# Kernel tuning notes

Hardware: AMD Instinct MI355X
Metric: run time of the kernel (lower is better)

## Reference

```python
import jax, jax.numpy as jnp
import numpy as np

EMBED_DIM = 1024
NUM_HEADS = 16
HEAD_DIM = EMBED_DIM // NUM_HEADS
EPSILON = 0.01
C = 2.0 + EPSILON
SCORE_SCALE = 1.0
B, L = 2, 2048


def setup_inputs() -> dict:
    key = jax.random.key(0)
    k0, k1, k2, k3, k4 = jax.random.split(key, 5)
    x = jax.random.normal(k0, (B, L, EMBED_DIM), dtype=jnp.float32)
    # flax Linear kernels: (in, out)
    W_qkv = jax.random.normal(k1, (EMBED_DIM, 3 * EMBED_DIM), dtype=jnp.float32) / np.sqrt(EMBED_DIM)
    b_qkv = jnp.zeros((3 * EMBED_DIM,), dtype=jnp.float32)
    W_out = jax.random.normal(k2, (EMBED_DIM, EMBED_DIM), dtype=jnp.float32) / np.sqrt(EMBED_DIM)
    b_out = jnp.zeros((EMBED_DIM,), dtype=jnp.float32)
    return {"x": x, "W_qkv": W_qkv, "b_qkv": b_qkv, "W_out": W_out, "b_out": b_out}


def reference(x, W_qkv, b_qkv, W_out, b_out):
    Bb, Ll, E = x.shape
    qkv = x @ W_qkv + b_qkv                      # [B, L, 3E]
    q, k, v = jnp.split(qkv, 3, axis=-1)
    def to_heads(t):
        return t.reshape(Bb, Ll, NUM_HEADS, HEAD_DIM).transpose(0, 2, 1, 3)  # [B,H,L,D]
    q, k, v = to_heads(q), to_heads(k), to_heads(v)
    q_norm = q / jnp.linalg.norm(q, axis=-1, keepdims=True)
    k_norm = k / jnp.linalg.norm(k, axis=-1, keepdims=True)
    x_dot = jnp.einsum('bhid,bhjd->bhij', q_norm, k_norm)   # [B,H,L,L]
    scores = (x_dot ** 2) / (C - 2.0 * x_dot) * SCORE_SCALE
    mask = jnp.triu(jnp.ones((Ll, Ll), dtype=scores.dtype), k=1) * -1e9
    scores = scores + mask[None, None, :, :]
    attn = jax.nn.softmax(scores, axis=-1)
    out = jnp.einsum('bhij,bhjd->bhid', attn, v)            # [B,H,L,D]
    out = out.transpose(0, 2, 1, 3).reshape(Bb, Ll, E)
    return out @ W_out + b_out
```

## Files before the change

### kernel.cpp

```cpp
#include <hip/hip_runtime.h>
#include <cstdint>
#include <cstddef>

#define B_DIM 2
#define L_DIM 2048
#define E_DIM 1024
#define H_DIM 16
#define HD    64
#define M_ROWS (B_DIM * L_DIM)
#define QKV_N  (3 * E_DIM)
#define C_CONST 2.01f
#define NCH_BH 40
#define LOG2E 1.4426950408889634f
#define LN2   0.6931471805599453f

typedef unsigned short ushort_t;
typedef __attribute__((ext_vector_type(8))) short bf16x8;
typedef __attribute__((ext_vector_type(4))) float f32x4;

__device__ __forceinline__ unsigned int f2bf(float f) {
    union { float f; unsigned int u; } v; v.f = f;
    return (v.u + 0x7FFFu + ((v.u >> 16) & 1u)) >> 16;
}
__device__ __forceinline__ float bf2f_lo(unsigned int u) {
    union { unsigned int u; float f; } v; v.u = u << 16; return v.f;
}
__device__ __forceinline__ float bf2f_hi(unsigned int u) {
    union { unsigned int u; float f; } v; v.u = u & 0xffff0000u; return v.f;
}

__device__ __forceinline__ void gload16(const void* g, void* l) {
    __builtin_amdgcn_global_load_lds(
        (const __attribute__((address_space(1))) void*)g,
        (__attribute__((address_space(3))) void*)l, 16, 0, 0);
}

__device__ __forceinline__ void transpose_tile_dev(
    const float* __restrict__ in, ushort_t* __restrict__ out,
    int R, int Cn, int c0, int r0, int tid, float t[64][65])
{
    for (int idx = tid; idx < 4096; idx += 256) {
        const int r = idx >> 6, c = idx & 63;
        t[r][c] = in[(size_t)(r0 + r) * Cn + c0 + c];
    }
    __syncthreads();
    for (int idx = tid; idx < 4096; idx += 256) {
        const int c = idx >> 6, r = idx & 63;
        out[(size_t)(c0 + c) * R + r0 + r] = (ushort_t)f2bf(t[r][c]);
    }
}

__global__ __launch_bounds__(256) void prep_kernel(
    const float* __restrict__ x, ushort_t* __restrict__ xb,
    const float* __restrict__ Wqkv, ushort_t* __restrict__ WqkvT,
    const float* __restrict__ Wout, ushort_t* __restrict__ WoutT)
{
    __shared__ float t[64][65];
    const int bx = blockIdx.x;
    const int tid = threadIdx.x;
    if (bx < 4096) {
        const int i = bx * 256 + tid;
        const float4 v = ((const float4*)x)[i];
        uint2 p;
        p.x = f2bf(v.x) | (f2bf(v.y) << 16);
        p.y = f2bf(v.z) | (f2bf(v.w) << 16);
        ((uint2*)xb)[i] = p;
    } else if (bx < 4096 + 768) {
        const int idx = bx - 4096;
        transpose_tile_dev(Wqkv, WqkvT, E_DIM, QKV_N, (idx % 48) * 64, (idx / 48) * 64, tid, t);
    } else {
        const int idx = bx - 4864;
        transpose_tile_dev(Wout, WoutT, E_DIM, E_DIM, (idx & 15) * 64, (idx >> 4) * 64, tid, t);
    }
}

template<int NCOLS, int MODE>
__global__ __launch_bounds__(256) void gemm_bt_kernel(
    const ushort_t* __restrict__ A, const ushort_t* __restrict__ BT,
    const float* __restrict__ bias, float* __restrict__ outf,
    ushort_t* __restrict__ q16, ushort_t* __restrict__ k16,
    ushort_t* __restrict__ v16)
{
    __shared__ __align__(16) ushort_t Abuf[128 * 32];
    __shared__ __align__(16) ushort_t Bbuf[128 * 32];
    const int tid = threadIdx.x;
    const int wave = tid >> 6, lane = tid & 63;
    const int m0 = blockIdx.x * 128, n0 = blockIdx.y * 128;
    const int wr = (wave >> 1) * 64, wc = (wave & 1) * 64;
    const int g = lane >> 4, l15 = lane & 15;

    f32x4 acc[4][4];
    #pragma unroll
    for (int i = 0; i < 4; ++i)
        #pragma unroll
        for (int j = 0; j < 4; ++j) acc[i][j] = f32x4{0.f, 0.f, 0.f, 0.f};

    const int sr = tid >> 2;
    const int sc = (tid & 3) * 8;
    const ushort_t* Asrc0 = A + (size_t)(m0 + sr) * 1024 + sc;
    const ushort_t* Asrc1 = A + (size_t)(m0 + 64 + sr) * 1024 + sc;
    const ushort_t* Bsrc0 = BT + (size_t)(n0 + sr) * 1024 + sc;
    const ushort_t* Bsrc1 = BT + (size_t)(n0 + 64 + sr) * 1024 + sc;
    ushort_t* Adst0 = &Abuf[tid * 8];
    ushort_t* Adst1 = &Abuf[2048 + tid * 8];
    ushort_t* Bdst0 = &Bbuf[tid * 8];
    ushort_t* Bdst1 = &Bbuf[2048 + tid * 8];

    for (int k0 = 0; k0 < 1024; k0 += 32) {
        __syncthreads();
        gload16(Asrc0 + k0, Adst0);
        gload16(Asrc1 + k0, Adst1);
        gload16(Bsrc0 + k0, Bdst0);
        gload16(Bsrc1 + k0, Bdst1);
        __syncthreads();

        bf16x8 af[4];
        #pragma unroll
        for (int mt = 0; mt < 4; ++mt)
            af[mt] = *(const bf16x8*)&Abuf[(wr + mt * 16 + l15) * 32 + 8 * g];
        #pragma unroll
        for (int nt = 0; nt < 4; ++nt) {
            const bf16x8 bfr = *(const bf16x8*)&Bbuf[(wc + nt * 16 + l15) * 32 + 8 * g];
            #pragma unroll
            for (int mt = 0; mt < 4; ++mt)
                acc[mt][nt] = __builtin_amdgcn_mfma_f32_16x16x32_bf16(af[mt], bfr, acc[mt][nt], 0, 0, 0);
        }
    }

    if (MODE == 0) {
        const int nBase = n0 + wc;
        const int sel = nBase >> 10;
        const int h   = (nBase & 1023) >> 6;
        float bv[4];
        #pragma unroll
        for (int nt = 0; nt < 4; ++nt) bv[nt] = bias[nBase + nt * 16 + l15];

        if (sel <= 1) {
            ushort_t* dst16 = (sel == 0) ? q16 : k16;
            #pragma unroll
            for (int mt = 0; mt < 4; ++mt) {
                float val[4][4], ss[4] = {0.f, 0.f, 0.f, 0.f};
                #pragma unroll
                for (int nt = 0; nt < 4; ++nt)
                    #pragma unroll
                    for (int r = 0; r < 4; ++r) {
                        const float v = acc[mt][nt][r] + bv[nt];
                        val[nt][r] = v;
                        ss[r] = fmaf(v, v, ss[r]);
                    }
                #pragma unroll
                for (int r = 0; r < 4; ++r) {
                    float t = ss[r];
                    t += __shfl_xor(t, 1); t += __shfl_xor(t, 2);
                    t += __shfl_xor(t, 4); t += __shfl_xor(t, 8);
                    ss[r] = 1.0f / sqrtf(t);
                }
                #pragma unroll
                for (int r = 0; r < 4; ++r) {
                    const int m = m0 + wr + mt * 16 + 4 * g + r;
                    const int bb = m >> 11, ll = m & 2047;
                    ushort_t* base = dst16 + ((size_t)((bb * H_DIM + h) * L_DIM + ll)) * HD + l15;
                    #pragma unroll
                    for (int nt = 0; nt < 4; ++nt)
                        base[nt * 16] = (ushort_t)f2bf(val[nt][r] * ss[r]);
                }
            }
        } else {
            #pragma unroll
            for (int mt = 0; mt < 4; ++mt)
                #pragma unroll
                for (int r = 0; r < 4; ++r) {
                    const int m = m0 + wr + mt * 16 + 4 * g + r;
                    const int bb = m >> 11, ll = m & 2047;
                    ushort_t* base = v16 + ((size_t)((bb * H_DIM + h) * L_DIM + ll)) * HD + l15;
                    #pragma unroll
                    for (int nt = 0; nt < 4; ++nt)
                        base[nt * 16] = (ushort_t)f2bf(acc[mt][nt][r] + bv[nt]);
                }
        }
    } else {
        #pragma unroll
        for (int nt = 0; nt < 4; ++nt) {
            const int n = n0 + wc + nt * 16 + l15;
            const float bvv = bias[n];
            #pragma unroll
            for (int mt = 0; mt < 4; ++mt)
                #pragma unroll
                for (int r = 0; r < 4; ++r) {
                    const int m = m0 + wr + mt * 16 + 4 * g + r;
                    outf[(size_t)m * E_DIM + n] = acc[mt][nt][r] + bvv;
                }
        }
    }
}

__global__ __launch_bounds__(256) void vt_transpose_kernel(
    const ushort_t* __restrict__ vb, ushort_t* __restrict__ vt)
{
    __shared__ ushort_t t[64][68];
    const int kt = blockIdx.x, bh = blockIdx.y;
    const int tid = threadIdx.x;
    const ushort_t* src = vb + ((size_t)bh * L_DIM + kt * 64) * HD;
    #pragma unroll
    for (int p = 0; p < 16; ++p) {
        const int idx = tid + 256 * p;
        t[idx >> 6][idx & 63] = src[idx];
    }
    __syncthreads();
    ushort_t* dst = vt + (size_t)bh * HD * L_DIM + kt * 64;
    #pragma unroll
    for (int p = 0; p < 16; ++p) {
        const int idx = tid + 256 * p;
        const int d = idx >> 6, k = idx & 63;
        dst[(size_t)d * L_DIM + k] = t[k][d];
    }
}

__global__ __launch_bounds__(512) void attn_mfma_kernel(
    const ushort_t* __restrict__ qn, const ushort_t* __restrict__ kn,
    const ushort_t* __restrict__ vt,
    ushort_t* __restrict__ pO, float* __restrict__ pl, float* __restrict__ pm)
{
    __shared__ __align__(16) ushort_t Qs[128 * 64];
    __shared__ __align__(16) ushort_t Ks[2][64 * 64];
    __shared__ __align__(16) ushort_t Vs[2][64 * 64];

    int c = blockIdx.x, qtp = 0, s = 0;
    #pragma unroll
    for (int gg = 0; gg < 4; ++gg) {
        const int sz = 4 * (gg + 1);
        if (c < sz) { qtp = 4 * gg + c / (gg + 1); s = c - (c / (gg + 1)) * (gg + 1); break; }
        c -= sz;
    }
    const int bh = blockIdx.y;
    const int cid = bh * NCH_BH + blockIdx.x;
    const int q0 = qtp * 128;
    const int kt0 = 8 * s;
    const int ktEnd = min(8 * s + 8, 2 * qtp + 2);

    const int tid = threadIdx.x, w = tid >> 6, lane = tid & 63;
    const int g = lane >> 4, l15 = lane & 15;
    ushort_t* Pw = &Qs[w * 16 * 64];

    const ushort_t* Qg = qn + ((size_t)bh * L_DIM + q0) * HD;
    const ushort_t* Kg = kn + (size_t)bh * L_DIM * HD;
    const ushort_t* Vg = vt + (size_t)bh * HD * L_DIM;

    const int srow = tid >> 3, sch = tid & 7;
    const int qr2 = (tid + 512) >> 3, qc2 = (tid + 512) & 7;

    {
        const int j0 = kt0 * 64;
        gload16(Qg + srow * 64 + ((sch ^ (srow & 7)) << 3), Qs + srow * 64 + (sch << 3));
        gload16(Qg + qr2 * 64 + ((qc2 ^ (qr2 & 7)) << 3), Qs + qr2 * 64 + (qc2 << 3));
        gload16(Kg + (size_t)(j0 + srow) * 64 + ((sch ^ (srow & 7)) << 3), Ks[0] + srow * 64 + (sch << 3));
        gload16(Vg + (size_t)srow * L_DIM + j0 + ((sch ^ (srow & 7)) << 3), Vs[0] + srow * 64 + (sch << 3));
    }
    __syncthreads();

    bf16x8 qf[2];
    #pragma unroll
    for (int kc = 0; kc < 2; ++kc) {
        const int row = 16 * w + l15;
        qf[kc] = *(const bf16x8*)&Qs[row * 64 + (((4 * kc + g) ^ (row & 7)) << 3)];
    }

    f32x4 o[4];
    float M = 8.0f * LOG2E, l_i = 0.f;
    #pragma unroll
    for (int j = 0; j < 4; ++j) o[j] = f32x4{0.f, 0.f, 0.f, 0.f};

    const int qrow = q0 + 16 * w + l15;

    for (int kt = kt0; kt < ktEnd; ++kt) {
        const int cur = (kt - kt0) & 1;
        if (kt + 1 < ktEnd) {
            const int j1 = (kt + 1) * 64;
            gload16(Kg + (size_t)(j1 + srow) * 64 + ((sch ^ (srow & 7)) << 3),
                    Ks[cur ^ 1] + srow * 64 + (sch << 3));
            gload16(Vg + (size_t)srow * L_DIM + j1 + ((sch ^ (srow & 7)) << 3),
                    Vs[cur ^ 1] + srow * 64 + (sch << 3));
        }
        const int j0 = kt * 64;

        bf16x8 ak[4][2];
        #pragma unroll
        for (int kt4 = 0; kt4 < 4; ++kt4)
            #pragma unroll
            for (int kc = 0; kc < 2; ++kc) {
                const int row = 16 * kt4 + l15;
                ak[kt4][kc] = *(const bf16x8*)&Ks[cur][row * 64 + (((4 * kc + g) ^ (row & 7)) << 3)];
            }
        f32x4 st[4];
        #pragma unroll
        for (int kt4 = 0; kt4 < 4; ++kt4) st[kt4] = f32x4{0.f, 0.f, 0.f, 0.f};
        __builtin_amdgcn_s_setprio(1);
        #pragma unroll
        for (int kc = 0; kc < 2; ++kc)
            #pragma unroll
            for (int kt4 = 0; kt4 < 4; ++kt4)
                st[kt4] = __builtin_amdgcn_mfma_f32_16x16x32_bf16(
                    ak[kt4][kc], qf[kc], st[kt4], 0, 0, 0);
        __builtin_amdgcn_s_setprio(0);

        const float negM = -M;
        float emax = -1e30f;
        #pragma unroll
        for (int kt4 = 0; kt4 < 4; ++kt4)
            #pragma unroll
            for (int r = 0; r < 4; ++r) {
                const float x = st[kt4][r];
                const float t = (x * x) * LOG2E;
                const float d = fmaf(-2.f, x, C_CONST);
                float rr;
                asm("v_rcp_f32 %0, %1" : "=v"(rr) : "v"(d));
                const float e = fmaf(t, rr, negM);
                st[kt4][r] = e;
                emax = fmaxf(emax, e);
            }

        if (kt >= 2 * qtp) {
            emax = -1e30f;
            #pragma unroll
            for (int kt4 = 0; kt4 < 4; ++kt4)
                #pragma unroll
                for (int r = 0; r < 4; ++r) {
                    const int key = j0 + 16 * kt4 + 4 * g + r;
                    float e = st[kt4][r];
                    e = (key > qrow) ? -100.f : e;
                    st[kt4][r] = e;
                    emax = fmaxf(emax, e);
                }
        }

        if (__any(emax > 0.f)) {
            float rm = fmaxf(emax, __shfl_xor(emax, 16));
            rm = fmaxf(rm, __shfl_xor(rm, 32));
            rm = fmaxf(rm, 0.f);
            #pragma unroll
            for (int kt4 = 0; kt4 < 4; ++kt4)
                #pragma unroll
                for (int r = 0; r < 4; ++r) st[kt4][r] -= rm;
            const float nrm = -rm;
            float scl;
            asm("v_exp_f32 %0, %1" : "=v"(scl) : "v"(nrm));
            l_i *= scl;
            #pragma unroll
            for (int r = 0; r < 4; ++r) {
                const float sv = __shfl(scl, 4 * g + r);
                #pragma unroll
                for (int dt = 0; dt < 4; ++dt) o[dt][r] *= sv;
            }
            M += rm;
        }

        float ts = 0.f;
        #pragma unroll
        for (int kt4 = 0; kt4 < 4; ++kt4) {
            const float e0 = st[kt4][0], e1 = st[kt4][1];
            const float e2 = st[kt4][2], e3 = st[kt4][3];
            float p0, p1, p2, p3;
            asm("v_exp_f32 %0, %1" : "=v"(p0) : "v"(e0));
            asm("v_exp_f32 %0, %1" : "=v"(p1) : "v"(e1));
            asm("v_exp_f32 %0, %1" : "=v"(p2) : "v"(e2));
            asm("v_exp_f32 %0, %1" : "=v"(p3) : "v"(e3));
            ts += (p0 + p1) + (p2 + p3);
            uint2 pk;
            asm("v_cvt_pk_bf16_f32 %0, %1, %2" : "=v"(pk.x) : "v"(p0), "v"(p1));
            asm("v_cvt_pk_bf16_f32 %0, %1, %2" : "=v"(pk.y) : "v"(p2), "v"(p3));
            const int ch = 2 * kt4 + (g >> 1);
            *(uint2*)&Pw[l15 * 64 + ((ch ^ (l15 & 7)) << 3) + 4 * (g & 1)] = pk;
        }
        l_i += ts;

        bf16x8 ap[2], av[4][2];
        #pragma unroll
        for (int kc = 0; kc < 2; ++kc)
            ap[kc] = *(const bf16x8*)&Pw[l15 * 64 + (((4 * kc + g) ^ (l15 & 7)) << 3)];
        #pragma unroll
        for (int dt = 0; dt < 4; ++dt)
            #pragma unroll
            for (int kc = 0; kc < 2; ++kc) {
                const int row = 16 * dt + l15;
                av[dt][kc] = *(const bf16x8*)&Vs[cur][row * 64 + (((4 * kc + g) ^ (row & 7)) << 3)];
            }
        __builtin_amdgcn_s_setprio(1);
        #pragma unroll
        for (int kc = 0; kc < 2; ++kc)
            #pragma unroll
            for (int dt = 0; dt < 4; ++dt)
                o[dt] = __builtin_amdgcn_mfma_f32_16x16x32_bf16(
                    ap[kc], av[dt][kc], o[dt], 0, 0, 0);
        __builtin_amdgcn_s_setprio(0);

        __syncthreads();
    }

    l_i += __shfl_xor(l_i, 16);
    l_i += __shfl_xor(l_i, 32);
    ushort_t* po = pO + (size_t)cid * 8192 + (16 * w) * 64;
    #pragma unroll
    for (int r = 0; r < 4; ++r)
        #pragma unroll
        for (int dt = 0; dt < 4; ++dt)
            po[(4 * g + r) * 64 + 16 * dt + l15] = (ushort_t)f2bf(o[dt][r]);
    if (lane < 16) {
        pl[cid * 128 + 16 * w + lane] = l_i;
        pm[cid * 128 + 16 * w + lane] = M * LN2;
    }
}

__global__ __launch_bounds__(256) void combine_kernel(
    const ushort_t* __restrict__ pO, const float* __restrict__ pl,
    const float* __restrict__ pm, ushort_t* __restrict__ cb)
{
    const int qt2 = blockIdx.x, bh = blockIdx.y;
    const int qtp = qt2 >> 1, half = qt2 & 1;
    const int gg = qtp >> 2, ns = gg + 1;
    const int cid0 = bh * NCH_BH + 2 * gg * (gg + 1) + (qtp & 3) * ns;
    const int tid = threadIdx.x;
    const int row = tid >> 2, seg = tid & 3;
    const int rowc = half * 64 + row;

    float mt = -1e30f;
    for (int s2 = 0; s2 < ns; ++s2)
        mt = fmaxf(mt, pm[(cid0 + s2) * 128 + rowc]);

    float acc[16];
    #pragma unroll
    for (int j = 0; j < 16; ++j) acc[j] = 0.f;
    float l_tot = 0.f;
    for (int s2 = 0; s2 < ns; ++s2) {
        const int cid = cid0 + s2;
        const float sc = __expf(pm[cid * 128 + rowc] - mt);
        l_tot += pl[cid * 128 + rowc] * sc;
        const ushort_t* src = pO + (size_t)cid * 8192 + rowc * 64 + seg * 16;
        const uint4 u0 = *(const uint4*)src;
        const uint4 u1 = *(const uint4*)(src + 8);
        const unsigned int uu[8] = {u0.x, u0.y, u0.z, u0.w, u1.x, u1.y, u1.z, u1.w};
        #pragma unroll
        for (int j = 0; j < 8; ++j) {
            acc[2 * j]     = fmaf(sc, bf2f_lo(uu[j]), acc[2 * j]);
            acc[2 * j + 1] = fmaf(sc, bf2f_hi(uu[j]), acc[2 * j + 1]);
        }
    }
    const float inv = 1.0f / l_tot;
    const int b = bh >> 4, h = bh & 15;
    ushort_t* dst = cb + ((size_t)(b * L_DIM + qt2 * 64 + row)) * E_DIM + h * HD + seg * 16;
    uint4 w0, w1;
    w0.x = f2bf(acc[0] * inv)  | (f2bf(acc[1] * inv) << 16);
    w0.y = f2bf(acc[2] * inv)  | (f2bf(acc[3] * inv) << 16);
    w0.z = f2bf(acc[4] * inv)  | (f2bf(acc[5] * inv) << 16);
    w0.w = f2bf(acc[6] * inv)  | (f2bf(acc[7] * inv) << 16);
    w1.x = f2bf(acc[8] * inv)  | (f2bf(acc[9] * inv) << 16);
    w1.y = f2bf(acc[10] * inv) | (f2bf(acc[11] * inv) << 16);
    w1.z = f2bf(acc[12] * inv) | (f2bf(acc[13] * inv) << 16);
    w1.w = f2bf(acc[14] * inv) | (f2bf(acc[15] * inv) << 16);
    *(uint4*)dst = w0;
    *(uint4*)(dst + 8) = w1;
}

extern "C" void kernel_launch(void* const* d_in, const int* in_sizes, int n_in,
                              void* d_out, int out_size, void* d_ws, size_t ws_size,
                              hipStream_t stream)
{
    const float* x    = (const float*)d_in[0];
    const float* Wqkv = (const float*)d_in[1];
    const float* bqkv = (const float*)d_in[2];
    const float* Wout = (const float*)d_in[3];
    const float* bout = (const float*)d_in[4];
    float* out = (float*)d_out;

    char* ws = (char*)d_ws;
    const size_t MB = 1u << 20;
    ushort_t* qn16  = (ushort_t*)(ws + 0 * MB);
    ushort_t* kn16  = (ushort_t*)(ws + 8 * MB);
    ushort_t* vb16  = (ushort_t*)(ws + 16 * MB);
    ushort_t* vt16  = (ushort_t*)(ws + 24 * MB);
    ushort_t* xb    = (ushort_t*)(ws + 32 * MB);
    ushort_t* cb    = (ushort_t*)(ws + 32 * MB);
    ushort_t* WqkvT = (ushort_t*)(ws + 40 * MB);
    ushort_t* pO    = (ushort_t*)(ws + 40 * MB);
    float*    pl    = (float*)   (ws + 60 * MB);
    float*    pm    = (float*)   (ws + 61 * MB);
    ushort_t* WoutT = (ushort_t*)(ws + 62 * MB);

    prep_kernel<<<5120, 256, 0, stream>>>(x, xb, Wqkv, WqkvT, Wout, WoutT);

    gemm_bt_kernel<QKV_N, 0><<<dim3(M_ROWS / 128, QKV_N / 128), 256, 0, stream>>>(
        xb, WqkvT, bqkv, nullptr, qn16, kn16, vb16);

    vt_transpose_kernel<<<dim3(L_DIM / 64, B_DIM * H_DIM), 256, 0, stream>>>(vb16, vt16);

    attn_mfma_kernel<<<dim3(NCH_BH, B_DIM * H_DIM), 512, 0, stream>>>(qn16, kn16, vt16, pO, pl, pm);

    combine_kernel<<<dim3(L_DIM / 64, B_DIM * H_DIM), 256, 0, stream>>>(pO, pl, pm, cb);

    gemm_bt_kernel<E_DIM, 1><<<dim3(M_ROWS / 128, E_DIM / 128), 256, 0, stream>>>(
        cb, WoutT, bout, out, nullptr, nullptr, nullptr);
}
```

Baseline: 122.8 us.

## Fuse V transpose into QKV GEMM epilogue and double-buffer GEMM LDS tiles

Result: slower. 133.3 us (+8.5%).

```diff
diff --git a/kernel.cpp b/kernel.cpp
--- a/kernel.cpp
+++ b/kernel.cpp
@@ -79,10 +79,10 @@
     const ushort_t* __restrict__ A, const ushort_t* __restrict__ BT,
     const float* __restrict__ bias, float* __restrict__ outf,
     ushort_t* __restrict__ q16, ushort_t* __restrict__ k16,
-    ushort_t* __restrict__ v16)
-{
-    __shared__ __align__(16) ushort_t Abuf[128 * 32];
-    __shared__ __align__(16) ushort_t Bbuf[128 * 32];
+    ushort_t* __restrict__ vt16)
+{
+    __shared__ __align__(16) ushort_t Abuf[2][128 * 32];
+    __shared__ __align__(16) ushort_t Bbuf[2][128 * 32];
     const int tid = threadIdx.x;
     const int wave = tid >> 6, lane = tid & 63;
     const int m0 = blockIdx.x * 128, n0 = blockIdx.y * 128;
@@ -101,30 +101,34 @@
     const ushort_t* Asrc1 = A + (size_t)(m0 + 64 + sr) * 1024 + sc;
     const ushort_t* Bsrc0 = BT + (size_t)(n0 + sr) * 1024 + sc;
     const ushort_t* Bsrc1 = BT + (size_t)(n0 + 64 + sr) * 1024 + sc;
-    ushort_t* Adst0 = &Abuf[tid * 8];
-    ushort_t* Adst1 = &Abuf[2048 + tid * 8];
-    ushort_t* Bdst0 = &Bbuf[tid * 8];
-    ushort_t* Bdst1 = &Bbuf[2048 + tid * 8];
+
+    gload16(Asrc0, &Abuf[0][tid * 8]);
+    gload16(Asrc1, &Abuf[0][2048 + tid * 8]);
+    gload16(Bsrc0, &Bbuf[0][tid * 8]);
+    gload16(Bsrc1, &Bbuf[0][2048 + tid * 8]);
+    __syncthreads();
 
     for (int k0 = 0; k0 < 1024; k0 += 32) {
-        __syncthreads();
-        gload16(Asrc0 + k0, Adst0);
-        gload16(Asrc1 + k0, Adst1);
-        gload16(Bsrc0 + k0, Bdst0);
-        gload16(Bsrc1 + k0, Bdst1);
-        __syncthreads();
+        const int cur = (k0 >> 5) & 1;
+        if (k0 + 32 < 1024) {
+            gload16(Asrc0 + k0 + 32, &Abuf[cur ^ 1][tid * 8]);
+            gload16(Asrc1 + k0 + 32, &Abuf[cur ^ 1][2048 + tid * 8]);
+            gload16(Bsrc0 + k0 + 32, &Bbuf[cur ^ 1][tid * 8]);
+            gload16(Bsrc1 + k0 + 32, &Bbuf[cur ^ 1][2048 + tid * 8]);
+        }
 
         bf16x8 af[4];
         #pragma unroll
         for (int mt = 0; mt < 4; ++mt)
-            af[mt] = *(const bf16x8*)&Abuf[(wr + mt * 16 + l15) * 32 + 8 * g];
+            af[mt] = *(const bf16x8*)&Abuf[cur][(wr + mt * 16 + l15) * 32 + 8 * g];
         #pragma unroll
         for (int nt = 0; nt < 4; ++nt) {
-            const bf16x8 bfr = *(const bf16x8*)&Bbuf[(wc + nt * 16 + l15) * 32 + 8 * g];
+            const bf16x8 bfr = *(const bf16x8*)&Bbuf[cur][(wc + nt * 16 + l15) * 32 + 8 * g];
             #pragma unroll
             for (int mt = 0; mt < 4; ++mt)
                 acc[mt][nt] = __builtin_amdgcn_mfma_f32_16x16x32_bf16(af[mt], bfr, acc[mt][nt], 0, 0, 0);
         }
+        __syncthreads();
     }
 
     if (MODE == 0) {
@@ -166,17 +170,24 @@
                 }
             }
         } else {
-            #pragma unroll
-            for (int mt = 0; mt < 4; ++mt)
-                #pragma unroll
-                for (int r = 0; r < 4; ++r) {
-                    const int m = m0 + wr + mt * 16 + 4 * g + r;
-                    const int bb = m >> 11, ll = m & 2047;
-                    ushort_t* base = v16 + ((size_t)((bb * H_DIM + h) * L_DIM + ll)) * HD + l15;
-                    #pragma unroll
-                    for (int nt = 0; nt < 4; ++nt)
-                        base[nt * 16] = (ushort_t)f2bf(acc[mt][nt][r] + bv[nt]);
+            const int bb = m0 >> 11;
+            #pragma unroll
+            for (int nt = 0; nt < 4; ++nt) {
+                const int d = nt * 16 + l15;
+                ushort_t* vbase = vt16 + ((size_t)((bb * H_DIM + h) * HD + d)) * L_DIM;
+                #pragma unroll
+                for (int mt = 0; mt < 4; ++mt) {
+                    const int key = (m0 & 2047) + wr + mt * 16 + 4 * g;
+                    const float v0 = acc[mt][nt][0] + bv[nt];
+                    const float v1 = acc[mt][nt][1] + bv[nt];
+                    const float v2 = acc[mt][nt][2] + bv[nt];
+                    const float v3 = acc[mt][nt][3] + bv[nt];
+                    uint2 pk;
+                    asm("v_cvt_pk_bf16_f32 %0, %1, %2" : "=v"(pk.x) : "v"(v0), "v"(v1));
+                    asm("v_cvt_pk_bf16_f32 %0, %1, %2" : "=v"(pk.y) : "v"(v2), "v"(v3));
+                    *(uint2*)&vbase[key] = pk;
                 }
+            }
         }
     } else {
         #pragma unroll
@@ -191,28 +202,6 @@
                     outf[(size_t)m * E_DIM + n] = acc[mt][nt][r] + bvv;
                 }
         }
-    }
-}
-
-__global__ __launch_bounds__(256) void vt_transpose_kernel(
-    const ushort_t* __restrict__ vb, ushort_t* __restrict__ vt)
-{
-    __shared__ ushort_t t[64][68];
-    const int kt = blockIdx.x, bh = blockIdx.y;
-    const int tid = threadIdx.x;
-    const ushort_t* src = vb + ((size_t)bh * L_DIM + kt * 64) * HD;
-    #pragma unroll
-    for (int p = 0; p < 16; ++p) {
-        const int idx = tid + 256 * p;
-        t[idx >> 6][idx & 63] = src[idx];
-    }
-    __syncthreads();
-    ushort_t* dst = vt + (size_t)bh * HD * L_DIM + kt * 64;
-    #pragma unroll
-    for (int p = 0; p < 16; ++p) {
-        const int idx = tid + 256 * p;
-        const int d = idx >> 6, k = idx & 63;
-        dst[(size_t)d * L_DIM + k] = t[k][d];
     }
 }
 
@@ -475,7 +464,6 @@
     const size_t MB = 1u << 20;
     ushort_t* qn16  = (ushort_t*)(ws + 0 * MB);
     ushort_t* kn16  = (ushort_t*)(ws + 8 * MB);
-    ushort_t* vb16  = (ushort_t*)(ws + 16 * MB);
     ushort_t* vt16  = (ushort_t*)(ws + 24 * MB);
     ushort_t* xb    = (ushort_t*)(ws + 32 * MB);
     ushort_t* cb    = (ushort_t*)(ws + 32 * MB);
@@ -488,9 +476,7 @@
     prep_kernel<<<5120, 256, 0, stream>>>(x, xb, Wqkv, WqkvT, Wout, WoutT);
 
     gemm_bt_kernel<QKV_N, 0><<<dim3(M_ROWS / 128, QKV_N / 128), 256, 0, stream>>>(
-        xb, WqkvT, bqkv, nullptr, qn16, kn16, vb16);
-
-    vt_transpose_kernel<<<dim3(L_DIM / 64, B_DIM * H_DIM), 256, 0, stream>>>(vb16, vt16);
+        xb, WqkvT, bqkv, nullptr, qn16, kn16, vt16);
 
     attn_mfma_kernel<<<dim3(NCH_BH, B_DIM * H_DIM), 512, 0, stream>>>(qn16, kn16, vt16, pO, pl, pm);
 
```
